# Performance work log

Measured on AMD Instinct MI355X. Metric: run time of the kernel, lower is better.

## Reference

```python
import jax, jax.numpy as jnp
import numpy as np
from jax import lax


def _gelu(x):
    return jax.nn.gelu(x, approximate=False)  # torch nn.GELU default = exact erf


def _ln_cf(x, g, b, eps=1e-6):
    # channels_first LayerNorm over dim 1 (biased variance, as in the source)
    m = x.mean(1, keepdims=True)
    v = ((x - m) ** 2).mean(1, keepdims=True)
    return g[None, :, None, None] * ((x - m) / jnp.sqrt(v + eps)) + b[None, :, None, None]


def _conv1x1(x, w):
    return jnp.einsum('bihw,oi->bohw', x, w[:, :, 0, 0])


def _conv3x3(x, w, d):
    # 3x3 conv, padding=dilation=d, no bias
    return lax.conv_general_dilated(x, w, (1, 1), [(d, d), (d, d)], rhs_dilation=(d, d),
                                    dimension_numbers=('NCHW', 'OIHW', 'NCHW'))


def _forward(x, conv1_w, conv1_b, conv2_w, conv2_b,
             cw_w1, cw_b1, cw_ln_g, cw_ln_b, cw_w2, cw_b2,
             aspp0_w, aspp0_g, aspp0_b, aspp1_w, aspp1_g, aspp1_b,
             aspp2_w, aspp2_g, aspp2_b, aspp3_w, aspp3_g, aspp3_b,
             asppp_w, asppp_g, asppp_b, proj_w, proj_g, proj_b):
    B, C, H, W = x.shape
    # x1 = conv1(x)
    x1 = _conv1x1(x, conv1_w) + conv1_b[None, :, None, None]
    # ChannelWeighting
    avg = x.mean((2, 3))                                    # [B,C]
    mx = x.max((2, 3))
    o = jnp.abs(avg - mx) * avg
    h = o @ cw_w1.T + cw_b1                                 # [B,Cout]
    mu = h.mean(-1, keepdims=True)
    vv = ((h - mu) ** 2).mean(-1, keepdims=True)
    h = cw_ln_g * ((h - mu) / jnp.sqrt(vv + 1e-5)) + cw_ln_b  # nn.LayerNorm eps=1e-5
    s = jax.nn.sigmoid(h @ cw_w2.T + cw_b2)                 # [B,C]
    xc = x * s[:, :, None, None] + x
    # ASPP (dropout in project is identity at eval)
    b0 = _gelu(_ln_cf(_conv1x1(xc, aspp0_w), aspp0_g, aspp0_b))
    b1 = _gelu(_ln_cf(_conv3x3(xc, aspp1_w, 3), aspp1_g, aspp1_b))
    b2 = _gelu(_ln_cf(_conv3x3(xc, aspp2_w, 6), aspp2_g, aspp2_b))
    b3 = _gelu(_ln_cf(_conv3x3(xc, aspp3_w, 9), aspp3_g, aspp3_b))
    gp = xc.mean((2, 3), keepdims=True)                     # AdaptiveAvgPool2d(1)
    bp = _gelu(_ln_cf(_conv1x1(gp, asppp_w), asppp_g, asppp_b))
    bp = jnp.broadcast_to(bp, (B, C, H, W))                 # bilinear 1x1->HxW == broadcast
    cat = jnp.concatenate([b0, b1, b2, b3, bp], axis=1)     # [B,5C,H,W]
    proj = _gelu(_ln_cf(_conv1x1(cat, proj_w), proj_g, proj_b))
    xa = _conv1x1(proj, conv1_w) + conv1_b[None, :, None, None]
    # AttentionModule, batched (redundant discarded Q@attn from source omitted)
    Co = xa.shape[1]
    HW = H * W
    P = x1.reshape(B, Co, HW)
    Q = xa.reshape(B, Co, HW)
    S = jnp.einsum('bcq,bcp->bqp', Q, P) / jnp.sqrt(jnp.asarray(HW, jnp.float32))
    A = jax.nn.softmax(S, axis=-1)                          # softmax over dim=1 of S[q,p] -> p
    L = jnp.einsum('bck,bkj->bcj', P, A).reshape(B, Co, H, W)
    O = L + xa
    return _conv1x1(O, conv2_w) + conv2_b[None, :, None, None]


def setup_inputs() -> dict:
    key = jax.random.key(0)
    ks = jax.random.split(key, 16)
    Cin, Cout, B, H, W = 256, 128, 4, 64, 64

    def nrm(k, shape, fan):
        return jax.random.normal(k, shape, jnp.float32) / np.float32(np.sqrt(fan))

    return {
        'x': jax.random.normal(ks[0], (B, Cin, H, W), jnp.float32),
        'conv1_w': nrm(ks[1], (Cout, Cin, 1, 1), Cin),
        'conv1_b': jnp.zeros((Cout,), jnp.float32),
        'conv2_w': nrm(ks[2], (Cin, Cout, 1, 1), Cout),
        'conv2_b': jnp.zeros((Cin,), jnp.float32),
        'cw_w1': nrm(ks[3], (Cout, Cin), Cin),
        'cw_b1': jnp.zeros((Cout,), jnp.float32),
        'cw_ln_g': jnp.ones((Cout,), jnp.float32),
        'cw_ln_b': jnp.zeros((Cout,), jnp.float32),
        'cw_w2': nrm(ks[4], (Cin, Cout), Cout),
        'cw_b2': jnp.zeros((Cin,), jnp.float32),
        'aspp0_w': nrm(ks[5], (Cin, Cin, 1, 1), Cin),
        'aspp0_g': jnp.ones((Cin,), jnp.float32),
        'aspp0_b': jnp.zeros((Cin,), jnp.float32),
        'aspp1_w': nrm(ks[6], (Cin, Cin, 3, 3), Cin * 9),
        'aspp1_g': jnp.ones((Cin,), jnp.float32),
        'aspp1_b': jnp.zeros((Cin,), jnp.float32),
        'aspp2_w': nrm(ks[7], (Cin, Cin, 3, 3), Cin * 9),
        'aspp2_g': jnp.ones((Cin,), jnp.float32),
        'aspp2_b': jnp.zeros((Cin,), jnp.float32),
        'aspp3_w': nrm(ks[8], (Cin, Cin, 3, 3), Cin * 9),
        'aspp3_g': jnp.ones((Cin,), jnp.float32),
        'aspp3_b': jnp.zeros((Cin,), jnp.float32),
        'asppp_w': nrm(ks[9], (Cin, Cin, 1, 1), Cin),
        'asppp_g': jnp.ones((Cin,), jnp.float32),
        'asppp_b': jnp.zeros((Cin,), jnp.float32),
        'proj_w': nrm(ks[10], (Cin, 5 * Cin, 1, 1), 5 * Cin),
        'proj_g': jnp.ones((Cin,), jnp.float32),
        'proj_b': jnp.zeros((Cin,), jnp.float32),
    }


def reference(x, conv1_w, conv1_b, conv2_w, conv2_b,
              cw_w1, cw_b1, cw_ln_g, cw_ln_b, cw_w2, cw_b2,
              aspp0_w, aspp0_g, aspp0_b, aspp1_w, aspp1_g, aspp1_b,
              aspp2_w, aspp2_g, aspp2_b, aspp3_w, aspp3_g, aspp3_b,
              asppp_w, asppp_g, asppp_b, proj_w, proj_g, proj_b):
    return _forward(x, conv1_w, conv1_b, conv2_w, conv2_b,
                    cw_w1, cw_b1, cw_ln_g, cw_ln_b, cw_w2, cw_b2,
                    aspp0_w, aspp0_g, aspp0_b, aspp1_w, aspp1_g, aspp1_b,
                    aspp2_w, aspp2_g, aspp2_b, aspp3_w, aspp3_g, aspp3_b,
                    asppp_w, asppp_g, asppp_b, proj_w, proj_g, proj_b)
```

## Files before the change

### kernel.cpp

```cpp
#include <hip/hip_runtime.h>
#include <hip/hip_bf16.h>
#include <math.h>

#define NB 4
#define CI 256
#define CO 128
#define HW 4096

typedef __attribute__((ext_vector_type(8))) short s8v;
typedef __attribute__((ext_vector_type(4))) short s4v;
typedef __attribute__((ext_vector_type(4))) float f4v;

__device__ __forceinline__ unsigned short f2bf(float f){
    __hip_bfloat16 h = __float2bfloat16(f);
    return *reinterpret_cast<unsigned short*>(&h);
}

__device__ __forceinline__ void lds_dma16(const void* g, void* l){
    __builtin_amdgcn_global_load_lds((const __attribute__((address_space(1))) unsigned int*)g,
                                     (__attribute__((address_space(3))) unsigned int*)l,
                                     16, 0, 0);
}

__device__ __forceinline__ float gelu_f(float x){
    float z  = x * 0.70710678118654752f;
    float az = fabsf(z);
    float tt = 1.f / (1.f + 0.3275911f * az);
    float poly = tt*(0.254829592f + tt*(-0.284496736f + tt*(1.421413741f +
                 tt*(-1.453152027f + tt*1.061405429f))));
    float erfv = 1.f - poly * __expf(-az*az);
    erfv = (z < 0.f) ? -erfv : erfv;
    return 0.5f * x * (1.f + erfv);
}

__global__ void k_pre(const float* __restrict__ x, float* __restrict__ avg, float* __restrict__ mx,
                      const float* __restrict__ c1, const float* __restrict__ a0,
                      const float* __restrict__ pj, const float* __restrict__ c2,
                      const float* __restrict__ d3, const float* __restrict__ d6,
                      const float* __restrict__ d9,
                      unsigned short* __restrict__ w_c1, unsigned short* __restrict__ w_a0,
                      unsigned short* __restrict__ w_pj, unsigned short* __restrict__ w_c2,
                      unsigned short* __restrict__ w_d3, unsigned short* __restrict__ w_d6,
                      unsigned short* __restrict__ w_d9){
    int blk = blockIdx.x;
    int t = threadIdx.x;
    if (blk < 1024){
        const float* p = x + (long long)blk * HW;
        float s = 0.f, m = -1e30f;
        for (int i = t; i < HW; i += 256){ float v = p[i]; s += v; m = fmaxf(m, v); }
        __shared__ float ss[256], sm[256];
        ss[t] = s; sm[t] = m; __syncthreads();
        for (int o = 128; o > 0; o >>= 1){
            if (t < o){ ss[t] += ss[t+o]; sm[t] = fmaxf(sm[t], sm[t+o]); }
            __syncthreads();
        }
        if (t == 0){ avg[blk] = ss[0] / (float)HW; mx[blk] = sm[0]; }
        return;
    }
    int i = (blk - 1024)*256 + t;
    if (i < 458752){
        if (i < 32768)        w_c1[i]        = f2bf(c1[i]);
        else if (i < 98304)   w_a0[i-32768]  = f2bf(a0[i-32768]);
        else if (i < 425984)  w_pj[i-98304]  = f2bf(pj[i-98304]);
        else                  w_c2[i-425984] = f2bf(c2[i-425984]);
    } else {
        int j = i - 458752;
        int which = j / 589824;
        int l = j - which*589824;
        int tap = l >> 16, rem = l & 65535, o = rem >> 8, ci = rem & 255;
        const float* src = (which==0) ? d3 : ((which==1) ? d6 : d9);
        unsigned short* dst = (which==0) ? w_d3 : ((which==1) ? w_d6 : w_d9);
        dst[l] = f2bf(src[o*2304 + ci*9 + tap]);
    }
}

__global__ void k_cw(const float* __restrict__ avg, const float* __restrict__ mx,
                     const float* __restrict__ w1, const float* __restrict__ b1,
                     const float* __restrict__ lng, const float* __restrict__ lnb,
                     const float* __restrict__ w2, const float* __restrict__ b2,
                     float* __restrict__ sv, float* __restrict__ gp,
                     float* __restrict__ zb){
    int b = blockIdx.x, t = threadIdx.x;
    if (b == 0) zb[t] = 0.f;
    __shared__ float o_s[256];
    __shared__ float h_s[128];
    __shared__ float stat[2];
    float a = avg[b*256 + t];
    o_s[t] = fabsf(a - mx[b*256 + t]) * a;
    __syncthreads();
    if (t < 128){
        float h = b1[t];
        for (int i = 0; i < 256; i++) h += o_s[i] * w1[t*256 + i];
        h_s[t] = h;
    }
    __syncthreads();
    if (t == 0){
        float s = 0.f, s2 = 0.f;
        for (int j = 0; j < 128; j++){ s += h_s[j]; s2 += h_s[j]*h_s[j]; }
        float mean = s / 128.f;
        float var  = s2 / 128.f - mean*mean;
        stat[0] = mean; stat[1] = rsqrtf(var + 1e-5f);
    }
    __syncthreads();
    if (t < 128) h_s[t] = lng[t] * ((h_s[t] - stat[0]) * stat[1]) + lnb[t];
    __syncthreads();
    float z = b2[t];
    for (int j = 0; j < 128; j++) z += h_s[j] * w2[t*128 + j];
    float sig = 1.f / (1.f + __expf(-z));
    sv[b*256 + t] = sig;
    gp[b*256 + t] = a * (1.f + sig);
}

__global__ void k_xT(const float* __restrict__ x, const float* __restrict__ sv,
                     unsigned short* __restrict__ xT, unsigned short* __restrict__ xcT){
    int b = blockIdx.z, c0 = blockIdx.y*64, h0 = blockIdx.x*64;
    __shared__ unsigned short T1[64][66], T2[64][66];
    int t = threadIdx.x;
    int hl = t & 63, cs = t >> 6;
    #pragma unroll
    for (int r = 0; r < 16; r++){
        int c = cs*16 + r;
        float v = x[((long long)b*256 + c0 + c)*HW + h0 + hl];
        float sc = 1.f + sv[b*256 + c0 + c];
        T1[c][hl] = f2bf(v);
        T2[c][hl] = f2bf(v*sc);
    }
    __syncthreads();
    int cl = t & 63, hs = t >> 6;
    #pragma unroll
    for (int r = 0; r < 16; r++){
        int h = hs*16 + r;
        long long o = ((long long)b*HW + h0 + h)*256 + c0 + cl;
        xT[o]  = T1[cl][h];
        xcT[o] = T2[cl][h];
    }
}

__device__ __forceinline__ void ln_epi32(f4v acc[2][2],
        int b, int n0, int w, int lane, int m, int q, int t,
        const float* Gs, const float* Bts,
        float (*Psum)[32], float (*Psq)[32], float* Mn, float* Iv,
        unsigned short* __restrict__ outT, int outPitch, int colOff){
    float ls[2], ls2[2];
    #pragma unroll
    for (int ct = 0; ct < 2; ct++){
        float s = 0.f, s2 = 0.f;
        #pragma unroll
        for (int ms = 0; ms < 2; ms++)
            #pragma unroll
            for (int r = 0; r < 4; r++){ float v = acc[ms][ct][r]; s += v; s2 += v*v; }
        ls[ct] = s; ls2[ct] = s2;
    }
    #pragma unroll
    for (int ct = 0; ct < 2; ct++){
        ls[ct]  += __shfl_xor(ls[ct], 16);  ls[ct]  += __shfl_xor(ls[ct], 32);
        ls2[ct] += __shfl_xor(ls2[ct], 16); ls2[ct] += __shfl_xor(ls2[ct], 32);
    }
    if (lane < 16){
        #pragma unroll
        for (int ct = 0; ct < 2; ct++){ Psum[w][ct*16+lane] = ls[ct]; Psq[w][ct*16+lane] = ls2[ct]; }
    }
    __syncthreads();
    if (t < 32){
        float s = 0.f, s2 = 0.f;
        #pragma unroll
        for (int ww = 0; ww < 8; ww++){ s += Psum[ww][t]; s2 += Psq[ww][t]; }
        float mean = s * (1.f/256.f);
        Mn[t] = mean;
        Iv[t] = rsqrtf(s2*(1.f/256.f) - mean*mean + 1e-6f);
    }
    __syncthreads();
    #pragma unroll
    for (int ct = 0; ct < 2; ct++){
        int p = ct*16 + m;
        float mean = Mn[p], inv = Iv[p];
        long long rowb = ((long long)b*HW + n0 + p)*outPitch + colOff;
        #pragma unroll
        for (int ms = 0; ms < 2; ms++){
            s4v o4;
            #pragma unroll
            for (int r = 0; r < 4; r++){
                int c = w*32 + ms*16 + q*4 + r;
                float h = Gs[c]*((acc[ms][ct][r] - mean)*inv) + Bts[c];
                o4[r] = (short)f2bf(gelu_f(h));
            }
            *(s4v*)(outT + rowb + w*32 + ms*16 + q*4) = o4;
        }
    }
}

__global__ __launch_bounds__(512, 4)
void k_aspp(const unsigned short* __restrict__ w_a0, const unsigned short* __restrict__ w_d3,
            const unsigned short* __restrict__ w_d6, const unsigned short* __restrict__ w_d9,
            const unsigned short* __restrict__ BT,
            const float* __restrict__ a0_g, const float* __restrict__ a0_b,
            const float* __restrict__ a1_g, const float* __restrict__ a1_b,
            const float* __restrict__ a2_g, const float* __restrict__ a2_b,
            const float* __restrict__ a3_g, const float* __restrict__ a3_b,
            const float* __restrict__ gp, const float* __restrict__ ap_w,
            const float* __restrict__ ap_g, const float* __restrict__ ap_b,
            const float* __restrict__ zbuf,
            unsigned short* __restrict__ catT){
    int br = blockIdx.y, b = blockIdx.z;
    int t = threadIdx.x;
    __shared__ __align__(16) unsigned short As[256*64];
    __shared__ __align__(16) unsigned short Bs[128*64];
    __shared__ float Gs[256], Bts[256];
    if (br == 4){
        int p0 = blockIdx.x*128;
        float* z_s = (float*)As;
        unsigned short* bp_s = As + 2048;
        float* stat = (float*)(As + 4096);
        if (t < 256){
            float z = 0.f;
            for (int c = 0; c < 256; c++) z += gp[b*256 + c] * ap_w[t*256 + c];
            z_s[t] = z;
        }
        __syncthreads();
        if (t == 0){
            float s = 0.f, s2 = 0.f;
            for (int c = 0; c < 256; c++){ s += z_s[c]; s2 += z_s[c]*z_s[c]; }
            float mean = s / 256.f, var = s2 / 256.f - mean*mean;
            stat[0] = mean; stat[1] = rsqrtf(var + 1e-6f);
        }
        __syncthreads();
        if (t < 256){
            float h = ap_g[t] * ((z_s[t] - stat[0]) * stat[1]) + ap_b[t];
            bp_s[t] = f2bf(gelu_f(h));
        }
        __syncthreads();
        for (int it = 0; it < 8; it++){
            int i = it*512 + t;
            int pl = i >> 5, cj = (i & 31) * 8;
            s8v v8;
            #pragma unroll
            for (int k2 = 0; k2 < 8; k2++) v8[k2] = (short)bp_s[cj + k2];
            *(s8v*)(catT + ((long long)b*HW + p0 + pl)*1280 + 1024 + cj) = v8;
        }
        return;
    }
    int n0 = blockIdx.x * 128;
    const unsigned short* BTb = BT + (long long)b*HW*256;
    const unsigned short* A  = (br==0) ? w_a0 : (br==1) ? w_d3 : (br==2) ? w_d6 : w_d9;
    const float* g   = (br==0) ? a0_g : (br==1) ? a1_g : (br==2) ? a2_g : a3_g;
    const float* bta = (br==0) ? a0_b : (br==1) ? a1_b : (br==2) ? a2_b : a3_b;
    int d    = (br==0) ? 0 : (br==1) ? 3 : (br==2) ? 6 : 9;
    int NS   = (br==0) ? 4 : 36;
    if (t < 256){ Gs[t] = g[t]; Bts[t] = bta[t]; }

    int w = t>>6, lane = t&63, m = lane&15, q = lane>>4;
    int wr = w>>1, wc = w&1;
    int rsw = m&7;
    int rl8 = lane>>3;
    int gch = (lane&7) ^ rl8;
    int aoff = rl8*256 + gch*8;
    int y0 = n0 >> 6;

    f4v acc[4][4];
    #pragma unroll
    for (int ms = 0; ms < 4; ms++)
        #pragma unroll
        for (int ct = 0; ct < 4; ct++){ f4v z = {0.f,0.f,0.f,0.f}; acc[ms][ct] = z; }

    for (int s = 0; s < NS; ++s){
        int tap = s>>2, kc = s&3;
        int dy = tap/3 - 1, dx = tap%3 - 1;
        const unsigned short* abase = A + tap*65536 + kc*64 + aoff;
        #pragma unroll
        for (int i = 0; i < 4; i++){
            int row0 = w*32 + i*8;
            lds_dma16(abase + row0*256, &As[row0*64]);
        }
        int xadd = rl8 + dx*d;
        #pragma unroll
        for (int i = 0; i < 2; i++){
            int bn0 = w*16 + i*8;
            int yy = y0 + (bn0>>6) + dy*d;
            int xs = (bn0 & 63) + xadd;
            const unsigned short* gsrc = ((unsigned)yy < 64u && (unsigned)xs < 64u)
                ? (BTb + (long long)(yy*64 + xs)*256 + kc*64 + gch*8)
                : (const unsigned short*)zbuf;
            lds_dma16(gsrc, &Bs[bn0*64]);
        }
        __syncthreads();
        #pragma unroll
        for (int ks = 0; ks < 2; ks++){
            s8v bfr[4];
            #pragma unroll
            for (int ct = 0; ct < 4; ct++)
                bfr[ct] = *(const s8v*)&Bs[(wc*64 + ct*16 + m)*64 + ((q + 4*ks) ^ rsw)*8];
            #pragma unroll
            for (int ms = 0; ms < 4; ms++){
                s8v afr = *(const s8v*)&As[(wr*64 + ms*16 + m)*64 + ((q + 4*ks) ^ rsw)*8];
                #pragma unroll
                for (int ct = 0; ct < 4; ct++)
                    acc[ms][ct] = __builtin_amdgcn_mfma_f32_16x16x32_bf16(afr, bfr[ct], acc[ms][ct], 0,0,0);
            }
        }
        __syncthreads();
    }
    float* Psum = (float*)Bs;
    float* Psq  = Psum + 512;
    float* Mn   = Psq  + 512;
    float* Iv   = Mn   + 128;
    #pragma unroll
    for (int ct = 0; ct < 4; ct++){
        float s = 0.f, s2 = 0.f;
        #pragma unroll
        for (int ms = 0; ms < 4; ms++)
            #pragma unroll
            for (int r = 0; r < 4; r++){ float v = acc[ms][ct][r]; s += v; s2 += v*v; }
        s  += __shfl_xor(s, 16);  s  += __shfl_xor(s, 32);
        s2 += __shfl_xor(s2, 16); s2 += __shfl_xor(s2, 32);
        if (lane < 16){
            Psum[wr*128 + wc*64 + ct*16 + lane] = s;
            Psq [wr*128 + wc*64 + ct*16 + lane] = s2;
        }
    }
    __syncthreads();
    if (t < 128){
        float s  = Psum[t] + Psum[128+t] + Psum[256+t] + Psum[384+t];
        float s2 = Psq [t] + Psq [128+t] + Psq [256+t] + Psq [384+t];
        float mean = s * (1.f/256.f);
        Mn[t] = mean;
        Iv[t] = rsqrtf(s2*(1.f/256.f) - mean*mean + 1e-6f);
    }
    __syncthreads();
    #pragma unroll
    for (int ct = 0; ct < 4; ct++){
        int p = wc*64 + ct*16 + m;
        float mean = Mn[p], inv = Iv[p];
        long long rowb = ((long long)b*HW + n0 + p)*1280 + br*256;
        #pragma unroll
        for (int ms = 0; ms < 4; ms++){
            s4v o4;
            #pragma unroll
            for (int r = 0; r < 4; r++){
                int c = wr*64 + ms*16 + q*4 + r;
                float h = Gs[c]*((acc[ms][ct][r] - mean)*inv) + Bts[c];
                o4[r] = (short)f2bf(gelu_f(h));
            }
            *(s4v*)(catT + rowb + wr*64 + ms*16 + q*4) = o4;
        }
    }
}

__global__ __launch_bounds__(512)
void k_branch1(const unsigned short* __restrict__ A, int K,
               const unsigned short* __restrict__ BT,
               const float* __restrict__ g, const float* __restrict__ beta,
               unsigned short* __restrict__ outT, int outPitch, int colOff){
    int b = blockIdx.y, n0 = blockIdx.x*32;
    const unsigned short* BTb = BT + (long long)b*HW*K;
    __shared__ __align__(16) unsigned short As[256*64];
    __shared__ __align__(16) unsigned short Bs[32*64];
    __shared__ float Psum[8][32], Psq[8][32], Mn[32], Iv[32];
    __shared__ float Gs[256], Bts[256];
    int t = threadIdx.x, w = t>>6, lane = t&63, m = lane&15, q = lane>>4;
    int rl8 = lane>>3, gch = (lane&7) ^ rl8, rsw = m&7;
    if (t < 256){ Gs[t] = g[t]; Bts[t] = beta[t]; }
    f4v acc[2][2];
    #pragma unroll
    for (int ms = 0; ms < 2; ms++)
        #pragma unroll
        for (int ct = 0; ct < 2; ct++){ f4v z = {0.f,0.f,0.f,0.f}; acc[ms][ct] = z; }
    for (int k0 = 0; k0 < K; k0 += 64){
        #pragma unroll
        for (int i = 0; i < 4; i++){
            int ar = w*32 + i*8;
            lds_dma16(A + (long long)(ar + rl8)*K + k0 + gch*8, &As[ar*64]);
        }
        if (w < 4){
            int brr = w*8;
            lds_dma16(BTb + (long long)(n0 + brr + rl8)*K + k0 + gch*8, &Bs[brr*64]);
        }
        __syncthreads();
        #pragma unroll
        for (int ks = 0; ks < 2; ks++){
            s8v bfr[2];
            #pragma unroll
            for (int ct = 0; ct < 2; ct++)
                bfr[ct] = *(const s8v*)&Bs[(ct*16 + m)*64 + ((q + 4*ks) ^ rsw)*8];
            #pragma unroll
            for (int ms = 0; ms < 2; ms++){
                s8v afr = *(const s8v*)&As[(w*32 + ms*16 + m)*64 + ((q + 4*ks) ^ rsw)*8];
                #pragma unroll
                for (int ct = 0; ct < 2; ct++)
                    acc[ms][ct] = __builtin_amdgcn_mfma_f32_16x16x32_bf16(afr, bfr[ct], acc[ms][ct], 0,0,0);
            }
        }
        __syncthreads();
    }
    ln_epi32(acc, b, n0, w, lane, m, q, t, Gs, Bts, Psum, Psq, Mn, Iv, outT, outPitch, colOff);
}

__global__ __launch_bounds__(256)
void k_conv1m(const unsigned short* __restrict__ A,
              const unsigned short* __restrict__ BT,
              const float* __restrict__ bias,
              unsigned short* __restrict__ outT,
              unsigned short* __restrict__ outC,
              float* __restrict__ outF){
    int b = blockIdx.y, n0 = blockIdx.x*32;
    const unsigned short* BTb = BT + (long long)b*HW*256;
    __shared__ unsigned short As[128][72];
    __shared__ unsigned short Bs[32][72];
    int t = threadIdx.x, w = t>>6, lane = t&63, m = lane&15, q = lane>>4;
    f4v acc[2][2];
    #pragma unroll
    for (int ms = 0; ms < 2; ms++)
        #pragma unroll
        for (int ct = 0; ct < 2; ct++){ f4v z = {0.f,0.f,0.f,0.f}; acc[ms][ct] = z; }
    for (int k0 = 0; k0 < 256; k0 += 64){
        __syncthreads();
        {   int r = t>>1, half = t&1;
            const uint4* src = (const uint4*)(A + (long long)r*256 + k0 + half*32);
            uint4* dst = (uint4*)&As[r][half*32];
            dst[0]=src[0]; dst[1]=src[1]; dst[2]=src[2]; dst[3]=src[3];
        }
        {   int n = t>>3, ch = t&7;
            *(uint4*)&Bs[n][ch*8] = *(const uint4*)(BTb + (long long)(n0+n)*256 + k0 + ch*8);
        }
        __syncthreads();
        #pragma unroll
        for (int ks = 0; ks < 2; ks++){
            s8v bfr[2];
            #pragma unroll
            for (int ct = 0; ct < 2; ct++) bfr[ct] = *(const s8v*)&Bs[ct*16+m][q*8+ks*32];
            #pragma unroll
            for (int ms = 0; ms < 2; ms++){
                s8v afr = *(const s8v*)&As[w*32 + ms*16 + m][q*8+ks*32];
                #pragma unroll
                for (int ct = 0; ct < 2; ct++)
                    acc[ms][ct] = __builtin_amdgcn_mfma_f32_16x16x32_bf16(afr, bfr[ct], acc[ms][ct], 0,0,0);
            }
        }
    }
    #pragma unroll
    for (int ct = 0; ct < 2; ct++){
        int p = n0 + ct*16 + m;
        #pragma unroll
        for (int ms = 0; ms < 2; ms++){
            s4v o4;
            float vals[4];
            #pragma unroll
            for (int r = 0; r < 4; r++){
                int c = w*32 + ms*16 + q*4 + r;
                vals[r] = acc[ms][ct][r] + bias[c];
                o4[r] = (short)f2bf(vals[r]);
            }
            *(s4v*)(outT + ((long long)b*HW + p)*128 + w*32 + ms*16 + q*4) = o4;
            if (outC){
                #pragma unroll
                for (int r = 0; r < 4; r++){
                    int c = w*32 + ms*16 + q*4 + r;
                    outC[((long long)b*128 + c)*HW + p] = (unsigned short)o4[r];
                }
            }
            if (outF){
                #pragma unroll
                for (int r = 0; r < 4; r++){
                    int c = w*32 + ms*16 + q*4 + r;
                    outF[((long long)b*128 + c)*HW + p] = vals[r];
                }
            }
        }
    }
}

__global__ __launch_bounds__(256)
void k_attn_stats3(const unsigned short* __restrict__ QT,
                   const unsigned short* __restrict__ PT,
                   float* __restrict__ lpart){
    int b = blockIdx.z, jc = blockIdx.y, k0 = blockIdx.x * 128;
    const unsigned short* QTb = QT + (long long)b * HW * CO;
    const unsigned short* PTb = PT + (long long)b * HW * CO;
    __shared__ unsigned short Ps[2][64][132];
    int t = threadIdx.x;
    int w = t >> 6, lane = t & 63, m = lane & 15, q = lane >> 4;
    s8v a[2][4];
    #pragma unroll
    for (int kh = 0; kh < 2; kh++)
        #pragma unroll
        for (int ks = 0; ks < 4; ks++)
            a[kh][ks] = *(const s8v*)(QTb + (long long)(k0 + kh*64 + w*16 + m) * CO + q*8 + ks*32);
    float rl[2][4];
    #pragma unroll
    for (int kh = 0; kh < 2; kh++)
        #pragma unroll
        for (int r = 0; r < 4; r++) rl[kh][r] = 0.f;
    const float scale = 0.015625f;
    int jbase = jc * 1024;
    int sr = t >> 2, sch = t & 3;
    uint4 pf[4];
    {   const uint4* src = (const uint4*)(PTb + (long long)(jbase + sr) * CO + sch * 32);
        #pragma unroll
        for (int i = 0; i < 4; i++) pf[i] = src[i];
    }
    for (int jt = 0; jt < 16; jt++){
        int cur = jt & 1;
        {   uint4* dst = (uint4*)&Ps[cur][sr][sch * 32];
            #pragma unroll
            for (int i = 0; i < 4; i++) dst[i] = pf[i];
        }
        __syncthreads();
        if (jt < 15){
            const uint4* src = (const uint4*)(PTb + (long long)(jbase + (jt+1)*64 + sr) * CO + sch * 32);
            #pragma unroll
            for (int i = 0; i < 4; i++) pf[i] = src[i];
        }
        #pragma unroll
        for (int kh = 0; kh < 2; kh++){
            float sv[4][4];
            #pragma unroll
            for (int ct = 0; ct < 4; ct++){
                f4v acc = {0.f,0.f,0.f,0.f};
                #pragma unroll
                for (int ks = 0; ks < 4; ks++){
                    s8v bv = *(const s8v*)&Ps[cur][ct*16 + m][q*8 + ks*32];
                    acc = __builtin_amdgcn_mfma_f32_16x16x32_bf16(a[kh][ks], bv, acc, 0, 0, 0);
                }
                #pragma unroll
                for (int r = 0; r < 4; r++) sv[ct][r] = acc[r] * scale;
            }
            #pragma unroll
            for (int r = 0; r < 4; r++){
                float se = __expf(sv[0][r]) + __expf(sv[1][r])
                         + __expf(sv[2][r]) + __expf(sv[3][r]);
                #pragma unroll
                for (int msk = 1; msk < 16; msk <<= 1) se += __shfl_xor(se, msk);
                rl[kh][r] += se;
            }
        }
    }
    if (m == 0){
        #pragma unroll
        for (int kh = 0; kh < 2; kh++)
            #pragma unroll
            for (int r = 0; r < 4; r++){
                int k = k0 + kh*64 + w*16 + q*4 + r;
                lpart[(long long)jc * (NB*HW) + (long long)b*HW + k] = rl[kh][r];
            }
    }
}

__global__ __launch_bounds__(256)
void k_attn_apply2(const unsigned short* __restrict__ QT,
                   const unsigned short* __restrict__ PT,
                   const unsigned short* __restrict__ Pb,
                   const float* __restrict__ lpart,
                   float* __restrict__ Lp){
    int b = blockIdx.z, kc = blockIdx.y, j0 = blockIdx.x * 64;
    const unsigned short* QTb = QT + (long long)b * HW * CO;
    const unsigned short* PTb = PT + (long long)b * HW * CO;
    const unsigned short* Pbb = Pb + (long long)b * CO * HW;
    __shared__ unsigned short Qks[64][136];
    __shared__ unsigned short Pcs[128][72];
    __shared__ unsigned short Et[64][72];
    __shared__ float Il[2048];
    int t = threadIdx.x;
    int w = t >> 6, lane = t & 63, m = lane & 15, q = lane >> 4;
    int kbase = kc * 2048;
    {
        #pragma unroll
        for (int r = 0; r < 8; r++){
            int kl = t*8 + r;
            long long gi = (long long)b*HW + kbase + kl;
            float l = lpart[gi] + lpart[gi+16384] + lpart[gi+32768] + lpart[gi+49152];
            Il[kl] = 1.f / l;
        }
    }
    {
        int r = t >> 2, ch = t & 3;
        const uint4* src = (const uint4*)(PTb + (long long)(j0 + r) * CO + ch * 32);
        uint4* dst = (uint4*)&Qks[r][ch * 32];
        #pragma unroll
        for (int i = 0; i < 4; i++) dst[i] = src[i];
    }
    __syncthreads();
    s8v bj[4][4];
    #pragma unroll
    for (int ct = 0; ct < 4; ct++)
        #pragma unroll
        for (int ks = 0; ks < 4; ks++)
            bj[ct][ks] = *(const s8v*)&Qks[ct*16 + m][q*8 + ks*32];
    f4v accL[2][4];
    #pragma unroll
    for (int mt = 0; mt < 2; mt++)
        #pragma unroll
        for (int ct = 0; ct < 4; ct++){ f4v z = {0.f,0.f,0.f,0.f}; accL[mt][ct] = z; }
    const float scale = 0.015625f;
    for (int kt = 0; kt < 32; kt++){
        int k0 = kbase + kt*64;
        __syncthreads();
        {
            int r = t >> 2, ch = t & 3;
            const uint4* src = (const uint4*)(QTb + (long long)(k0 + r) * CO + ch * 32);
            uint4* dst = (uint4*)&Qks[r][ch * 32];
            #pragma unroll
            for (int i = 0; i < 4; i++) dst[i] = src[i];
        }
        {
            int c = t >> 1, hf = t & 1;
            const uint4* src = (const uint4*)(Pbb + (long long)c * HW + k0 + hf * 32);
            uint4* dst = (uint4*)&Pcs[c][hf * 32];
            #pragma unroll
            for (int i = 0; i < 4; i++) dst[i] = src[i];
        }
        __syncthreads();
        s8v aS[4];
        #pragma unroll
        for (int ks = 0; ks < 4; ks++) aS[ks] = *(const s8v*)&Qks[w*16 + m][q*8 + ks*32];
        float il[4];
        #pragma unroll
        for (int r = 0; r < 4; r++) il[r] = Il[kt*64 + w*16 + q*4 + r];
        #pragma unroll
        for (int ct = 0; ct < 4; ct++){
            f4v s = {0.f,0.f,0.f,0.f};
            #pragma unroll
            for (int ks = 0; ks < 4; ks++)
                s = __builtin_amdgcn_mfma_f32_16x16x32_bf16(aS[ks], bj[ct][ks], s, 0, 0, 0);
            s4v e4;
            #pragma unroll
            for (int r = 0; r < 4; r++)
                e4[r] = (short)f2bf(__expf(s[r]*scale) * il[r]);
            *(s4v*)&Et[ct*16 + m][w*16 + q*4] = e4;
        }
        __syncthreads();
        s8v aP[2][2];
        #pragma unroll
        for (int mt = 0; mt < 2; mt++)
            #pragma unroll
            for (int ks2 = 0; ks2 < 2; ks2++)
                aP[mt][ks2] = *(const s8v*)&Pcs[w*32 + mt*16 + m][q*8 + ks2*32];
        #pragma unroll
        for (int ct = 0; ct < 4; ct++){
            s8v bE0 = *(const s8v*)&Et[ct*16 + m][q*8];
            s8v bE1 = *(const s8v*)&Et[ct*16 + m][q*8 + 32];
            #pragma unroll
            for (int mt = 0; mt < 2; mt++){
                accL[mt][ct] = __builtin_amdgcn_mfma_f32_16x16x32_bf16(aP[mt][0], bE0, accL[mt][ct], 0, 0, 0);
                accL[mt][ct] = __builtin_amdgcn_mfma_f32_16x16x32_bf16(aP[mt][1], bE1, accL[mt][ct], 0, 0, 0);
            }
        }
    }
    float* Lpb = Lp + ((long long)(kc*NB + b) * CO) * HW;
    #pragma unroll
    for (int mt = 0; mt < 2; mt++)
        #pragma unroll
        for (int ct = 0; ct < 4; ct++)
            #pragma unroll
            for (int r = 0; r < 4; r++){
                int c = w*32 + mt*16 + q*4 + r;
                Lpb[(long long)c*HW + j0 + ct*16 + m] = accL[mt][ct][r];
            }
}

__global__ __launch_bounds__(256)
void k_outfused(const unsigned short* __restrict__ A,
                const float* __restrict__ Lp, const float* __restrict__ xa,
                const float* __restrict__ bias, float* __restrict__ out){
    int b = blockIdx.y, j0 = blockIdx.x*32;
    __shared__ unsigned short Bs[32][136];
    __shared__ __align__(16) char pool[256*68*2];
    int t = threadIdx.x;
    {
        float* Bsf = (float*)pool;
        int c = t>>1, jh = t&1;
        long long base = ((long long)b*CO + c)*HW + j0 + jh*16;
        const long long csz = (long long)NB*CO*HW;
        float v[16];
        #pragma unroll
        for (int r = 0; r < 16; r++) v[r] = xa[base + r];
        #pragma unroll
        for (int pidx = 0; pidx < 2; pidx++){
            const float* src = Lp + pidx*csz + base;
            #pragma unroll
            for (int r = 0; r < 16; r++) v[r] += src[r];
        }
        #pragma unroll
        for (int r = 0; r < 16; r++) Bsf[c*33 + jh*16 + r] = v[r];
    }
    __syncthreads();
    {
        const float* Bsf = (const float*)pool;
        int j = t>>3, cs = t&7;
        #pragma unroll
        for (int r = 0; r < 16; r++){
            int c = cs*16 + r;
            Bs[j][c] = f2bf(Bsf[c*33 + j]);
        }
    }
    __syncthreads();
    unsigned short (*As)[68] = (unsigned short(*)[68])pool;
    int w = t>>6, lane = t&63, m = lane&15, q = lane>>4;
    f4v acc[4][2];
    #pragma unroll
    for (int ms = 0; ms < 4; ms++)
        #pragma unroll
        for (int ct = 0; ct < 2; ct++){ f4v z = {0.f,0.f,0.f,0.f}; acc[ms][ct] = z; }
    for (int k0 = 0; k0 < 128; k0 += 64){
        __syncthreads();
        {   const uint4* src = (const uint4*)(A + (long long)t*128 + k0);
            uint4* dst = (uint4*)&As[t][0];
            #pragma unroll
            for (int i = 0; i < 8; i++) dst[i] = src[i];
        }
        __syncthreads();
        #pragma unroll
        for (int ks = 0; ks < 2; ks++){
            s8v bfr[2];
            #pragma unroll
            for (int ct = 0; ct < 2; ct++) bfr[ct] = *(const s8v*)&Bs[ct*16+m][k0 + ks*32 + q*8];
            #pragma unroll
            for (int ms = 0; ms < 4; ms++){
                s8v afr = *(const s8v*)&As[w*64 + ms*16 + m][q*8 + ks*32];
                #pragma unroll
                for (int ct = 0; ct < 2; ct++)
                    acc[ms][ct] = __builtin_amdgcn_mfma_f32_16x16x32_bf16(afr, bfr[ct], acc[ms][ct], 0,0,0);
            }
        }
    }
    #pragma unroll
    for (int ct = 0; ct < 2; ct++){
        int p = j0 + ct*16 + m;
        #pragma unroll
        for (int ms = 0; ms < 4; ms++)
            #pragma unroll
            for (int r = 0; r < 4; r++){
                int c = w*64 + ms*16 + q*4 + r;
                out[((long long)b*256 + c)*HW + p] = acc[ms][ct][r] + bias[c];
            }
    }
}

extern "C" void kernel_launch(void* const* d_in, const int* in_sizes, int n_in,
                              void* d_out, int out_size, void* d_ws, size_t ws_size,
                              hipStream_t stream) {
    const float* x       = (const float*)d_in[0];
    const float* conv1_w = (const float*)d_in[1];
    const float* conv1_b = (const float*)d_in[2];
    const float* conv2_w = (const float*)d_in[3];
    const float* conv2_b = (const float*)d_in[4];
    const float* cw_w1   = (const float*)d_in[5];
    const float* cw_b1   = (const float*)d_in[6];
    const float* cw_g    = (const float*)d_in[7];
    const float* cw_bt   = (const float*)d_in[8];
    const float* cw_w2   = (const float*)d_in[9];
    const float* cw_b2   = (const float*)d_in[10];
    const float* a0_w    = (const float*)d_in[11];
    const float* a0_g    = (const float*)d_in[12];
    const float* a0_b    = (const float*)d_in[13];
    const float* a1_w    = (const float*)d_in[14];
    const float* a1_g    = (const float*)d_in[15];
    const float* a1_b    = (const float*)d_in[16];
    const float* a2_w    = (const float*)d_in[17];
    const float* a2_g    = (const float*)d_in[18];
    const float* a2_b    = (const float*)d_in[19];
    const float* a3_w    = (const float*)d_in[20];
    const float* a3_g    = (const float*)d_in[21];
    const float* a3_b    = (const float*)d_in[22];
    const float* ap_w    = (const float*)d_in[23];
    const float* ap_g    = (const float*)d_in[24];
    const float* ap_b    = (const float*)d_in[25];
    const float* pj_w    = (const float*)d_in[26];
    const float* pj_g    = (const float*)d_in[27];
    const float* pj_b    = (const float*)d_in[28];
    float* out = (float*)d_out;

    float* ws    = (float*)d_ws;
    float* avg   = ws;
    float* mx    = ws + 1024;
    float* sv    = ws + 2048;
    float* gp    = ws + 3072;
    float* zbuf  = ws + 4096;
    float* xa    = ws + 37888;
    float* lpart = xa + 2097152;
    unsigned short* sb = (unsigned short*)(ws + 4232192);
    unsigned short* xT    = sb;
    unsigned short* xcT   = sb + 4194304;
    unsigned short* catT  = sb + 8388608;
    unsigned short* projT = sb + 29360128;
    unsigned short* P_bf  = sb + 33554432;
    unsigned short* PT_bf = sb + 35651584;
    unsigned short* QT_bf = sb + 37748736;
    unsigned short* w_c1  = sb + 41943040;
    unsigned short* w_a0  = sb + 41975808;
    unsigned short* w_pj  = sb + 42041344;
    unsigned short* w_c2  = sb + 42369024;
    unsigned short* w_d3  = sb + 42401792;
    unsigned short* w_d6  = sb + 42991616;
    unsigned short* w_d9  = sb + 43581440;
    float* Lp = (float*)catT;

    k_pre<<<dim3(9728), 256, 0, stream>>>(x, avg, mx,
                                          conv1_w, a0_w, pj_w, conv2_w, a1_w, a2_w, a3_w,
                                          w_c1, w_a0, w_pj, w_c2, w_d3, w_d6, w_d9);
    k_cw<<<dim3(NB), 256, 0, stream>>>(avg, mx, cw_w1, cw_b1, cw_g, cw_bt, cw_w2, cw_b2, sv, gp, zbuf);

    k_xT<<<dim3(64, 4, NB), 256, 0, stream>>>(x, sv, xT, xcT);

    k_conv1m<<<dim3(128, NB), 256, 0, stream>>>(w_c1, xT, conv1_b, PT_bf, P_bf, nullptr);

    k_aspp<<<dim3(32, 5, NB), 512, 0, stream>>>(w_a0, w_d3, w_d6, w_d9, xcT,
                                                a0_g, a0_b, a1_g, a1_b, a2_g, a2_b, a3_g, a3_b,
                                                gp, ap_w, ap_g, ap_b, zbuf, catT);

    k_branch1<<<dim3(128, NB), 512, 0, stream>>>(w_pj, 1280, catT, pj_g, pj_b, projT, 256, 0);

    k_conv1m<<<dim3(128, NB), 256, 0, stream>>>(w_c1, projT, conv1_b, QT_bf, nullptr, xa);

    k_attn_stats3<<<dim3(32, 4, NB), 256, 0, stream>>>(QT_bf, PT_bf, lpart);
    k_attn_apply2<<<dim3(64, 2, NB), 256, 0, stream>>>(QT_bf, PT_bf, P_bf, lpart, Lp);

    k_outfused<<<dim3(128, NB), 256, 0, stream>>>(w_c2, Lp, xa, conv2_b, out);

    (void)in_sizes; (void)n_in; (void)out_size; (void)ws_size;
}
```

Before: 397.7 us.

## Load GEMM tiles via direct global-to-LDS DMA with XOR-swizzled layouts

Replaces register-staged global-to-LDS copies in the conv1 GEMM, the attention-apply kernel and the final projection GEMM with global_load_lds 16-byte DMA transfers. The padded LDS arrays become unpadded tiles with an XOR chunk swizzle so fragment reads stay bank-conflict free. The aim is to cut VGPR traffic and instruction count on the load path. In exchange, the swizzle indexing has to be correct for every wave's row mapping, and the DMA writes must finish before the barrier that guards the LDS reads.

```diff
diff --git a/kernel.cpp b/kernel.cpp
--- a/kernel.cpp
+++ b/kernel.cpp
@@ -403,38 +403,38 @@
               float* __restrict__ outF){
     int b = blockIdx.y, n0 = blockIdx.x*32;
     const unsigned short* BTb = BT + (long long)b*HW*256;
-    __shared__ unsigned short As[128][72];
-    __shared__ unsigned short Bs[32][72];
+    __shared__ __align__(16) unsigned short As[128*64];
+    __shared__ __align__(16) unsigned short Bs[32*64];
     int t = threadIdx.x, w = t>>6, lane = t&63, m = lane&15, q = lane>>4;
+    int rl8 = lane>>3, gch = (lane&7) ^ rl8, rsw = m&7;
     f4v acc[2][2];
     #pragma unroll
     for (int ms = 0; ms < 2; ms++)
         #pragma unroll
         for (int ct = 0; ct < 2; ct++){ f4v z = {0.f,0.f,0.f,0.f}; acc[ms][ct] = z; }
     for (int k0 = 0; k0 < 256; k0 += 64){
-        __syncthreads();
-        {   int r = t>>1, half = t&1;
-            const uint4* src = (const uint4*)(A + (long long)r*256 + k0 + half*32);
-            uint4* dst = (uint4*)&As[r][half*32];
-            dst[0]=src[0]; dst[1]=src[1]; dst[2]=src[2]; dst[3]=src[3];
-        }
-        {   int n = t>>3, ch = t&7;
-            *(uint4*)&Bs[n][ch*8] = *(const uint4*)(BTb + (long long)(n0+n)*256 + k0 + ch*8);
-        }
+        #pragma unroll
+        for (int i = 0; i < 4; i++){
+            int ar = w*32 + i*8;
+            lds_dma16(A + (long long)(ar + rl8)*256 + k0 + gch*8, &As[ar*64]);
+        }
+        lds_dma16(BTb + (long long)(n0 + w*8 + rl8)*256 + k0 + gch*8, &Bs[w*8*64]);
         __syncthreads();
         #pragma unroll
         for (int ks = 0; ks < 2; ks++){
             s8v bfr[2];
             #pragma unroll
-            for (int ct = 0; ct < 2; ct++) bfr[ct] = *(const s8v*)&Bs[ct*16+m][q*8+ks*32];
+            for (int ct = 0; ct < 2; ct++)
+                bfr[ct] = *(const s8v*)&Bs[(ct*16 + m)*64 + ((q + 4*ks) ^ rsw)*8];
             #pragma unroll
             for (int ms = 0; ms < 2; ms++){
-                s8v afr = *(const s8v*)&As[w*32 + ms*16 + m][q*8+ks*32];
+                s8v afr = *(const s8v*)&As[(w*32 + ms*16 + m)*64 + ((q + 4*ks) ^ rsw)*8];
                 #pragma unroll
                 for (int ct = 0; ct < 2; ct++)
                     acc[ms][ct] = __builtin_amdgcn_mfma_f32_16x16x32_bf16(afr, bfr[ct], acc[ms][ct], 0,0,0);
             }
         }
+        __syncthreads();
     }
     #pragma unroll
     for (int ct = 0; ct < 2; ct++){
@@ -554,13 +554,16 @@
     const unsigned short* QTb = QT + (long long)b * HW * CO;
     const unsigned short* PTb = PT + (long long)b * HW * CO;
     const unsigned short* Pbb = Pb + (long long)b * CO * HW;
-    __shared__ unsigned short Qks[64][136];
-    __shared__ unsigned short Pcs[128][72];
+    __shared__ __align__(16) unsigned short Qks[64*128];
+    __shared__ __align__(16) unsigned short Pcs[128*64];
     __shared__ unsigned short Et[64][72];
     __shared__ float Il[2048];
     int t = threadIdx.x;
     int w = t >> 6, lane = t & 63, m = lane & 15, q = lane >> 4;
     int kbase = kc * 2048;
+    int rl4 = lane >> 4;
+    int rl8 = lane >> 3;
+    int gch8 = (lane & 7) ^ rl8;
     {
         #pragma unroll
         for (int r = 0; r < 8; r++){
@@ -571,11 +574,12 @@
         }
     }
     {
-        int r = t >> 2, ch = t & 3;
-        const uint4* src = (const uint4*)(PTb + (long long)(j0 + r) * CO + ch * 32);
-        uint4* dst = (uint4*)&Qks[r][ch * 32];
-        #pragma unroll
-        for (int i = 0; i < 4; i++) dst[i] = src[i];
+        #pragma unroll
+        for (int i = 0; i < 4; i++){
+            int rowb = w*16 + i*4;
+            int gch = (lane & 15) ^ ((rowb & 15) + rl4);
+            lds_dma16(PTb + (long long)(j0 + rowb + rl4)*CO + gch*8, &Qks[rowb*128]);
+        }
     }
     __syncthreads();
     s8v bj[4][4];
@@ -583,7 +587,7 @@
     for (int ct = 0; ct < 4; ct++)
         #pragma unroll
         for (int ks = 0; ks < 4; ks++)
-            bj[ct][ks] = *(const s8v*)&Qks[ct*16 + m][q*8 + ks*32];
+            bj[ct][ks] = *(const s8v*)&Qks[(ct*16 + m)*128 + ((q + 4*ks) ^ m)*8];
     f4v accL[2][4];
     #pragma unroll
     for (int mt = 0; mt < 2; mt++)
@@ -594,23 +598,25 @@
         int k0 = kbase + kt*64;
         __syncthreads();
         {
-            int r = t >> 2, ch = t & 3;
-            const uint4* src = (const uint4*)(QTb + (long long)(k0 + r) * CO + ch * 32);
-            uint4* dst = (uint4*)&Qks[r][ch * 32];
-            #pragma unroll
-            for (int i = 0; i < 4; i++) dst[i] = src[i];
+            #pragma unroll
+            for (int i = 0; i < 4; i++){
+                int rowb = w*16 + i*4;
+                int gch = (lane & 15) ^ ((rowb & 15) + rl4);
+                lds_dma16(QTb + (long long)(k0 + rowb + rl4)*CO + gch*8, &Qks[rowb*128]);
+            }
         }
         {
-            int c = t >> 1, hf = t & 1;
-            const uint4* src = (const uint4*)(Pbb + (long long)c * HW + k0 + hf * 32);
-            uint4* dst = (uint4*)&Pcs[c][hf * 32];
-            #pragma unroll
-            for (int i = 0; i < 4; i++) dst[i] = src[i];
+            #pragma unroll
+            for (int i = 0; i < 4; i++){
+                int rowb = w*32 + i*8;
+                lds_dma16(Pbb + (long long)(rowb + rl8)*HW + k0 + gch8*8, &Pcs[rowb*64]);
+            }
         }
         __syncthreads();
         s8v aS[4];
         #pragma unroll
-        for (int ks = 0; ks < 4; ks++) aS[ks] = *(const s8v*)&Qks[w*16 + m][q*8 + ks*32];
+        for (int ks = 0; ks < 4; ks++)
+            aS[ks] = *(const s8v*)&Qks[(w*16 + m)*128 + ((q + 4*ks) ^ m)*8];
         float il[4];
         #pragma unroll
         for (int r = 0; r < 4; r++) il[r] = Il[kt*64 + w*16 + q*4 + r];
@@ -632,7 +638,7 @@
         for (int mt = 0; mt < 2; mt++)
             #pragma unroll
             for (int ks2 = 0; ks2 < 2; ks2++)
-                aP[mt][ks2] = *(const s8v*)&Pcs[w*32 + mt*16 + m][q*8 + ks2*32];
+                aP[mt][ks2] = *(const s8v*)&Pcs[(w*32 + mt*16 + m)*64 + ((q + 4*ks2) ^ (m&7))*8];
         #pragma unroll
         for (int ct = 0; ct < 4; ct++){
             s8v bE0 = *(const s8v*)&Et[ct*16 + m][q*8];
@@ -692,8 +698,9 @@
         }
     }
     __syncthreads();
-    unsigned short (*As)[68] = (unsigned short(*)[68])pool;
+    unsigned short* As = (unsigned short*)pool;
     int w = t>>6, lane = t&63, m = lane&15, q = lane>>4;
+    int rl8 = lane>>3, gch = (lane&7) ^ rl8, rsw = m&7;
     f4v acc[4][2];
     #pragma unroll
     for (int ms = 0; ms < 4; ms++)
@@ -701,10 +708,10 @@
         for (int ct = 0; ct < 2; ct++){ f4v z = {0.f,0.f,0.f,0.f}; acc[ms][ct] = z; }
     for (int k0 = 0; k0 < 128; k0 += 64){
         __syncthreads();
-        {   const uint4* src = (const uint4*)(A + (long long)t*128 + k0);
-            uint4* dst = (uint4*)&As[t][0];
-            #pragma unroll
-            for (int i = 0; i < 8; i++) dst[i] = src[i];
+        #pragma unroll
+        for (int i = 0; i < 8; i++){
+            int ar = w*64 + i*8;
+            lds_dma16(A + (long long)(ar + rl8)*128 + k0 + gch*8, &As[ar*64]);
         }
         __syncthreads();
         #pragma unroll
@@ -714,7 +721,7 @@
             for (int ct = 0; ct < 2; ct++) bfr[ct] = *(const s8v*)&Bs[ct*16+m][k0 + ks*32 + q*8];
             #pragma unroll
             for (int ms = 0; ms < 4; ms++){
-                s8v afr = *(const s8v*)&As[w*64 + ms*16 + m][q*8 + ks*32];
+                s8v afr = *(const s8v*)&As[(w*64 + ms*16 + m)*64 + ((q + 4*ks) ^ rsw)*8];
                 #pragma unroll
                 for (int ct = 0; ct < 2; ct++)
                     acc[ms][ct] = __builtin_amdgcn_mfma_f32_16x16x32_bf16(afr, bfr[ct], acc[ms][ct], 0,0,0);
```

New measurement: 391.1 us. Within noise of the previous version (-1.7%).
